# Performance work log

Measured on AMD Instinct MI355X. Metric: run time of the kernel, lower is better.

Reference implementation:

```python
import jax, jax.numpy as jnp
import numpy as np

B, L, E, D = 4, 2048, 512, 128


def setup_inputs() -> dict:
    key = jax.random.key(0)
    k1, k2 = jax.random.split(key)
    emb_sentences = jax.random.normal(k1, (B, L, E), dtype=jnp.float32)
    # torch nn.Linear weight layout: [out_dim, in_dim]
    W = jax.random.normal(k2, (D, E), dtype=jnp.float32) * (1.0 / np.sqrt(E))
    return {"emb_sentences": emb_sentences, "W": W}


def reference(emb_sentences, W):
    # dep_embeddings = Linear(emb) with no bias: [B, L, D]
    dep = jnp.einsum('ble,de->bld', emb_sentences, W)
    # All-pairs squared Euclidean distances without the O(L^2 * D)
    # broadcast intermediate: ||xi - xj||^2 = ||xi||^2 + ||xj||^2 - 2 xi.xj
    sq = jnp.sum(dep * dep, axis=-1)                 # [B, L]
    gram = jnp.einsum('bid,bjd->bij', dep, dep)      # [B, L, L]
    distances = sq[:, :, None] + sq[:, None, :] - 2.0 * gram
    return dep, distances
```

## Files before the change

### kernel.cpp

```cpp
#include <hip/hip_runtime.h>
#include <hip/hip_bf16.h>


typedef __attribute__((ext_vector_type(8))) short  short8;
typedef __attribute__((ext_vector_type(4))) float  floatx4;

#define B_  4
#define L_  2048
#define E_  512
#define D_  128
#define M_  (B_*L_)

__device__ __forceinline__ unsigned short f2bf(float x) {
    union { float f; unsigned u; } v; v.f = x;
    unsigned r = v.u + 0x7FFF + ((v.u >> 16) & 1);
    return (unsigned short)(r >> 16);
}

__global__ __launch_bounds__(256)
void kA(const float* __restrict__ emb, const float* __restrict__ W,
        float* __restrict__ dep_out, unsigned short* __restrict__ dep_b16)
{
    __shared__ __align__(16) unsigned short As[128][40];
    __shared__ __align__(16) unsigned short Bs[128][40];

    const int tid  = threadIdx.x;
    const int lane = tid & 63;
    const int wave = tid >> 6;
    const int wr = wave >> 1, wc = wave & 1;
    const int l15 = lane & 15, lg = lane >> 4;
    const long m0 = (long)blockIdx.x * 128;

    floatx4 acc[4][4];
    #pragma unroll
    for (int i = 0; i < 4; ++i)
        #pragma unroll
        for (int j = 0; j < 4; ++j)
            acc[i][j] = (floatx4){0.f, 0.f, 0.f, 0.f};

    for (int k0 = 0; k0 < E_; k0 += 32) {
        #pragma unroll
        for (int jj = 0; jj < 4; ++jj) {
            int chunk = tid + 256 * jj;
            int row = chunk >> 3, c4 = chunk & 7;
            float4 va = *reinterpret_cast<const float4*>(emb + (m0 + row) * E_ + k0 + c4 * 4);
            ushort4 ua;
            ua.x = f2bf(va.x); ua.y = f2bf(va.y); ua.z = f2bf(va.z); ua.w = f2bf(va.w);
            *reinterpret_cast<ushort4*>(&As[row][c4 * 4]) = ua;
            float4 vb = *reinterpret_cast<const float4*>(W + row * E_ + k0 + c4 * 4);
            ushort4 ub;
            ub.x = f2bf(vb.x); ub.y = f2bf(vb.y); ub.z = f2bf(vb.z); ub.w = f2bf(vb.w);
            *reinterpret_cast<ushort4*>(&Bs[row][c4 * 4]) = ub;
        }
        __syncthreads();

        short8 af[4], bfr[4];
        #pragma unroll
        for (int mi = 0; mi < 4; ++mi)
            af[mi] = *reinterpret_cast<const short8*>(&As[wr * 64 + mi * 16 + l15][lg * 8]);
        #pragma unroll
        for (int ni = 0; ni < 4; ++ni)
            bfr[ni] = *reinterpret_cast<const short8*>(&Bs[wc * 64 + ni * 16 + l15][lg * 8]);
        #pragma unroll
        for (int mi = 0; mi < 4; ++mi)
            #pragma unroll
            for (int ni = 0; ni < 4; ++ni)
                acc[mi][ni] = __builtin_amdgcn_mfma_f32_16x16x32_bf16(
                    af[mi], bfr[ni], acc[mi][ni], 0, 0, 0);
        __syncthreads();
    }

    #pragma unroll
    for (int mi = 0; mi < 4; ++mi) {
        #pragma unroll
        for (int j = 0; j < 4; ++j) {
            long row = m0 + wr * 64 + mi * 16 + lg * 4 + j;
            #pragma unroll
            for (int ni = 0; ni < 4; ++ni) {
                int col = wc * 64 + ni * 16 + l15;
                float v = acc[mi][ni][j];
                dep_out[row * D_ + col] = v;
                dep_b16[row * D_ + col] = f2bf(v);
            }
        }
    }
}

__global__ __launch_bounds__(256)
void kSQ(const unsigned short* __restrict__ dep_b16, float* __restrict__ sq)
{
    int row  = blockIdx.x * 4 + (threadIdx.x >> 6);
    int lane = threadIdx.x & 63;
    unsigned v = *reinterpret_cast<const unsigned*>(dep_b16 + (long)row * D_ + lane * 2);
    union { unsigned u; float f; } a, b;
    a.u = v << 16; b.u = v & 0xFFFF0000u;
    float s = a.f * a.f + b.f * b.f;
    #pragma unroll
    for (int off = 32; off; off >>= 1) s += __shfl_down(s, off);
    if (lane == 0) sq[row] = s;
}

__global__ __launch_bounds__(256)
void kB(const unsigned short* __restrict__ dep_b16, const float* __restrict__ sq,
        float* __restrict__ dist)
{
    __shared__ __align__(16) unsigned short Is[128][136];
    __shared__ __align__(16) unsigned short Js[128][136];

    const int tid  = threadIdx.x;
    const int lane = tid & 63;
    const int wave = tid >> 6;
    const int wr = wave >> 1, wc = wave & 1;
    const int l15 = lane & 15, lg = lane >> 4;
    const int b  = blockIdx.z;
    const int i0 = blockIdx.y * 128;
    const int j0 = blockIdx.x * 128;
    const unsigned short* depb = dep_b16 + (long)b * L_ * D_;

    #pragma unroll
    for (int jj = 0; jj < 8; ++jj) {
        int chunk = tid + 256 * jj;
        int row = chunk >> 4, c8 = chunk & 15;
        short8 vi = *reinterpret_cast<const short8*>(depb + (long)(i0 + row) * D_ + c8 * 8);
        *reinterpret_cast<short8*>(&Is[row][c8 * 8]) = vi;
        short8 vj = *reinterpret_cast<const short8*>(depb + (long)(j0 + row) * D_ + c8 * 8);
        *reinterpret_cast<short8*>(&Js[row][c8 * 8]) = vj;
    }
    __syncthreads();

    floatx4 acc[4][4];
    #pragma unroll
    for (int i = 0; i < 4; ++i)
        #pragma unroll
        for (int j = 0; j < 4; ++j)
            acc[i][j] = (floatx4){0.f, 0.f, 0.f, 0.f};

    #pragma unroll
    for (int kk = 0; kk < 4; ++kk) {
        short8 af[4], bfr[4];
        #pragma unroll
        for (int mi = 0; mi < 4; ++mi)
            af[mi] = *reinterpret_cast<const short8*>(&Is[wr * 64 + mi * 16 + l15][kk * 32 + lg * 8]);
        #pragma unroll
        for (int ni = 0; ni < 4; ++ni)
            bfr[ni] = *reinterpret_cast<const short8*>(&Js[wc * 64 + ni * 16 + l15][kk * 32 + lg * 8]);
        #pragma unroll
        for (int mi = 0; mi < 4; ++mi)
            #pragma unroll
            for (int ni = 0; ni < 4; ++ni)
                acc[mi][ni] = __builtin_amdgcn_mfma_f32_16x16x32_bf16(
                    af[mi], bfr[ni], acc[mi][ni], 0, 0, 0);
    }

    const float* sqb = sq + b * L_;
    float sqc[4];
    #pragma unroll
    for (int ni = 0; ni < 4; ++ni)
        sqc[ni] = sqb[j0 + wc * 64 + ni * 16 + l15];

    float* db = dist + (long)b * L_ * L_;
    #pragma unroll
    for (int mi = 0; mi < 4; ++mi) {
        #pragma unroll
        for (int j = 0; j < 4; ++j) {
            int row = i0 + wr * 64 + mi * 16 + lg * 4 + j;
            float sr = sqb[row];
            #pragma unroll
            for (int ni = 0; ni < 4; ++ni) {
                int col = j0 + wc * 64 + ni * 16 + l15;
                db[(long)row * L_ + col] = sr + sqc[ni] - 2.0f * acc[mi][ni][j];
            }
        }
    }
}

extern "C" void kernel_launch(void* const* d_in, const int* in_sizes, int n_in,
                              void* d_out, int out_size, void* d_ws, size_t ws_size,
                              hipStream_t stream)
{
    const float* emb = (const float*)d_in[0];
    const float* W   = (const float*)d_in[1];

    float* dep_out = (float*)d_out;
    float* dist    = dep_out + (size_t)M_ * D_;

    unsigned short* dep_b16 = (unsigned short*)d_ws;
    float* sq = (float*)((char*)d_ws + (size_t)M_ * D_ * sizeof(unsigned short));

    hipLaunchKernelGGL(kA,  dim3(M_ / 128), dim3(256), 0, stream, emb, W, dep_out, dep_b16);
    hipLaunchKernelGGL(kSQ, dim3(M_ / 4),   dim3(256), 0, stream, dep_b16, sq);
    hipLaunchKernelGGL(kB,  dim3(L_ / 128, L_ / 128, B_), dim3(256), 0, stream,
                       dep_b16, sq, dist);
}
```

Before: 45.56 us.

## Drop LDS staging in both GEMMs, pre-convert W to bf16, shrink kA tiles

Adds a small kernel that converts W to bf16 once per call. The projection GEMM now uses 32-row tiles (more blocks) and loads MFMA fragments straight from global memory into registers with no LDS or barriers. The gram kernel also drops its LDS staging and reads bf16 fragments directly from global memory, relying on the L1/L2 caches for reuse. This removes shared-memory traffic and synchronisation, at the cost of more redundant global loads, less coalesced access patterns and one extra kernel launch.

```diff
diff --git a/kernel.cpp b/kernel.cpp
--- a/kernel.cpp
+++ b/kernel.cpp
@@ -18,66 +18,70 @@
 }
 
 __global__ __launch_bounds__(256)
-void kA(const float* __restrict__ emb, const float* __restrict__ W,
+void kW(const float* __restrict__ W, unsigned short* __restrict__ Wb)
+{
+    int i = (blockIdx.x * 256 + threadIdx.x) * 4;
+    float4 v = *reinterpret_cast<const float4*>(W + i);
+    ushort4 u;
+    u.x = f2bf(v.x); u.y = f2bf(v.y); u.z = f2bf(v.z); u.w = f2bf(v.w);
+    *reinterpret_cast<ushort4*>(Wb + i) = u;
+}
+
+__global__ __launch_bounds__(256)
+void kA(const float* __restrict__ emb, const unsigned short* __restrict__ Wb,
         float* __restrict__ dep_out, unsigned short* __restrict__ dep_b16)
 {
-    __shared__ __align__(16) unsigned short As[128][40];
-    __shared__ __align__(16) unsigned short Bs[128][40];
+    const int lane = threadIdx.x & 63;
+    const int wave = threadIdx.x >> 6;
+    const int l15 = lane & 15, lg = lane >> 4;
+    const long m0 = (long)blockIdx.x * 32;
 
-    const int tid  = threadIdx.x;
-    const int lane = tid & 63;
-    const int wave = tid >> 6;
-    const int wr = wave >> 1, wc = wave & 1;
-    const int l15 = lane & 15, lg = lane >> 4;
-    const long m0 = (long)blockIdx.x * 128;
-
-    floatx4 acc[4][4];
+    floatx4 acc[2][2];
     #pragma unroll
-    for (int i = 0; i < 4; ++i)
+    for (int i = 0; i < 2; ++i)
         #pragma unroll
-        for (int j = 0; j < 4; ++j)
+        for (int j = 0; j < 2; ++j)
             acc[i][j] = (floatx4){0.f, 0.f, 0.f, 0.f};
 
+    const float* a0 = emb + (m0 + l15) * E_;
+    const float* a1 = emb + (m0 + 16 + l15) * E_;
+    const unsigned short* b0 = Wb + (wave * 32 + l15) * E_;
+    const unsigned short* b1 = Wb + (wave * 32 + 16 + l15) * E_;
+
+    #pragma unroll
     for (int k0 = 0; k0 < E_; k0 += 32) {
+        const int kc = k0 + lg * 8;
+        short8 af[2], bf[2];
         #pragma unroll
-        for (int jj = 0; jj < 4; ++jj) {
-            int chunk = tid + 256 * jj;
-            int row = chunk >> 3, c4 = chunk & 7;
-            float4 va = *reinterpret_cast<const float4*>(emb + (m0 + row) * E_ + k0 + c4 * 4);
-            ushort4 ua;
-            ua.x = f2bf(va.x); ua.y = f2bf(va.y); ua.z = f2bf(va.z); ua.w = f2bf(va.w);
-            *reinterpret_cast<ushort4*>(&As[row][c4 * 4]) = ua;
-            float4 vb = *reinterpret_cast<const float4*>(W + row * E_ + k0 + c4 * 4);
-            ushort4 ub;
-            ub.x = f2bf(vb.x); ub.y = f2bf(vb.y); ub.z = f2bf(vb.z); ub.w = f2bf(vb.w);
-            *reinterpret_cast<ushort4*>(&Bs[row][c4 * 4]) = ub;
+        for (int mi = 0; mi < 2; ++mi) {
+            const float* ap = (mi == 0 ? a0 : a1) + kc;
+            float4 x = *reinterpret_cast<const float4*>(ap);
+            float4 y = *reinterpret_cast<const float4*>(ap + 4);
+            short8 t;
+            t[0] = (short)f2bf(x.x); t[1] = (short)f2bf(x.y);
+            t[2] = (short)f2bf(x.z); t[3] = (short)f2bf(x.w);
+            t[4] = (short)f2bf(y.x); t[5] = (short)f2bf(y.y);
+            t[6] = (short)f2bf(y.z); t[7] = (short)f2bf(y.w);
+            af[mi] = t;
         }
-        __syncthreads();
-
-        short8 af[4], bfr[4];
+        bf[0] = *reinterpret_cast<const short8*>(b0 + kc);
+        bf[1] = *reinterpret_cast<const short8*>(b1 + kc);
         #pragma unroll
-        for (int mi = 0; mi < 4; ++mi)
-            af[mi] = *reinterpret_cast<const short8*>(&As[wr * 64 + mi * 16 + l15][lg * 8]);
-        #pragma unroll
-        for (int ni = 0; ni < 4; ++ni)
-            bfr[ni] = *reinterpret_cast<const short8*>(&Bs[wc * 64 + ni * 16 + l15][lg * 8]);
-        #pragma unroll
-        for (int mi = 0; mi < 4; ++mi)
+        for (int mi = 0; mi < 2; ++mi)
             #pragma unroll
-            for (int ni = 0; ni < 4; ++ni)
+            for (int ni = 0; ni < 2; ++ni)
                 acc[mi][ni] = __builtin_amdgcn_mfma_f32_16x16x32_bf16(
-                    af[mi], bfr[ni], acc[mi][ni], 0, 0, 0);
-        __syncthreads();
+                    af[mi], bf[ni], acc[mi][ni], 0, 0, 0);
     }
 
     #pragma unroll
-    for (int mi = 0; mi < 4; ++mi) {
+    for (int mi = 0; mi < 2; ++mi) {
         #pragma unroll
         for (int j = 0; j < 4; ++j) {
-            long row = m0 + wr * 64 + mi * 16 + lg * 4 + j;
+            long row = m0 + mi * 16 + lg * 4 + j;
             #pragma unroll
-            for (int ni = 0; ni < 4; ++ni) {
-                int col = wc * 64 + ni * 16 + l15;
+            for (int ni = 0; ni < 2; ++ni) {
+                int col = wave * 32 + ni * 16 + l15;
                 float v = acc[mi][ni][j];
                 dep_out[row * D_ + col] = v;
                 dep_b16[row * D_ + col] = f2bf(v);
@@ -104,9 +108,6 @@
 void kB(const unsigned short* __restrict__ dep_b16, const float* __restrict__ sq,
         float* __restrict__ dist)
 {
-    __shared__ __align__(16) unsigned short Is[128][136];
-    __shared__ __align__(16) unsigned short Js[128][136];
-
     const int tid  = threadIdx.x;
     const int lane = tid & 63;
     const int wave = tid >> 6;
@@ -117,17 +118,6 @@
     const int j0 = blockIdx.x * 128;
     const unsigned short* depb = dep_b16 + (long)b * L_ * D_;
 
-    #pragma unroll
-    for (int jj = 0; jj < 8; ++jj) {
-        int chunk = tid + 256 * jj;
-        int row = chunk >> 4, c8 = chunk & 15;
-        short8 vi = *reinterpret_cast<const short8*>(depb + (long)(i0 + row) * D_ + c8 * 8);
-        *reinterpret_cast<short8*>(&Is[row][c8 * 8]) = vi;
-        short8 vj = *reinterpret_cast<const short8*>(depb + (long)(j0 + row) * D_ + c8 * 8);
-        *reinterpret_cast<short8*>(&Js[row][c8 * 8]) = vj;
-    }
-    __syncthreads();
-
     floatx4 acc[4][4];
     #pragma unroll
     for (int i = 0; i < 4; ++i)
@@ -135,21 +125,25 @@
         for (int j = 0; j < 4; ++j)
             acc[i][j] = (floatx4){0.f, 0.f, 0.f, 0.f};
 
+    const unsigned short* ibase = depb + (long)(i0 + wr * 64 + l15) * D_;
+    const unsigned short* jbase = depb + (long)(j0 + wc * 64 + l15) * D_;
+
     #pragma unroll
     for (int kk = 0; kk < 4; ++kk) {
-        short8 af[4], bfr[4];
+        const int kc = kk * 32 + lg * 8;
+        short8 af[4], bf[4];
         #pragma unroll
         for (int mi = 0; mi < 4; ++mi)
-            af[mi] = *reinterpret_cast<const short8*>(&Is[wr * 64 + mi * 16 + l15][kk * 32 + lg * 8]);
+            af[mi] = *reinterpret_cast<const short8*>(ibase + (long)mi * 16 * D_ + kc);
         #pragma unroll
         for (int ni = 0; ni < 4; ++ni)
-            bfr[ni] = *reinterpret_cast<const short8*>(&Js[wc * 64 + ni * 16 + l15][kk * 32 + lg * 8]);
+            bf[ni] = *reinterpret_cast<const short8*>(jbase + (long)ni * 16 * D_ + kc);
         #pragma unroll
         for (int mi = 0; mi < 4; ++mi)
             #pragma unroll
             for (int ni = 0; ni < 4; ++ni)
                 acc[mi][ni] = __builtin_amdgcn_mfma_f32_16x16x32_bf16(
-                    af[mi], bfr[ni], acc[mi][ni], 0, 0, 0);
+                    af[mi], bf[ni], acc[mi][ni], 0, 0, 0);
     }
 
     const float* sqb = sq + b * L_;
@@ -185,10 +179,14 @@
     float* dist    = dep_out + (size_t)M_ * D_;
 
     unsigned short* dep_b16 = (unsigned short*)d_ws;
-    float* sq = (float*)((char*)d_ws + (size_t)M_ * D_ * sizeof(unsigned short));
+    float* sq  = (float*)((char*)d_ws + (size_t)M_ * D_ * sizeof(unsigned short));
+    unsigned short* Wb = (unsigned short*)((char*)d_ws
+                         + (size_t)M_ * D_ * sizeof(unsigned short)
+                         + (size_t)M_ * sizeof(float));
 
-    hipLaunchKernelGGL(kA,  dim3(M_ / 128), dim3(256), 0, stream, emb, W, dep_out, dep_b16);
-    hipLaunchKernelGGL(kSQ, dim3(M_ / 4),   dim3(256), 0, stream, dep_b16, sq);
+    hipLaunchKernelGGL(kW,  dim3((D_ * E_) / (256 * 4)), dim3(256), 0, stream, W, Wb);
+    hipLaunchKernelGGL(kA,  dim3(M_ / 32), dim3(256), 0, stream, emb, Wb, dep_out, dep_b16);
+    hipLaunchKernelGGL(kSQ, dim3(M_ / 4),  dim3(256), 0, stream, dep_b16, sq);
     hipLaunchKernelGGL(kB,  dim3(L_ / 128, L_ / 128, B_), dim3(256), 0, stream,
                        dep_b16, sq, dist);
 }
```

Result: slower. 51.69 us (+13.5%).

## Fuse projection, norms and distance GEMM into one cooperative persistent kernel

Applied to the files above, without the earlier changes.

Replaces the three separate launches with one cooperative kernel of 512 blocks. Phase one computes a 16-row projection tile per block straight from global memory without LDS staging and folds the squared-norm reduction into its epilogue. A grid-wide sync follows, after which each block computes two 128x128 distance tiles. The aim is to remove launch gaps and the separate norm kernel, at the cost of a grid barrier, lower per-block reuse in the projection, and a fallback two-kernel path if the cooperative launch fails.

```diff
diff --git a/kernel.cpp b/kernel.cpp
--- a/kernel.cpp
+++ b/kernel.cpp
@@ -1,5 +1,8 @@
 #include <hip/hip_runtime.h>
 #include <hip/hip_bf16.h>
+#include <hip/hip_cooperative_groups.h>
+
+namespace cg = cooperative_groups;
 
 
 typedef __attribute__((ext_vector_type(8))) short  short8;
@@ -10,26 +13,105 @@
 #define E_  512
 #define D_  128
 #define M_  (B_*L_)
-
-__device__ __forceinline__ unsigned short f2bf(float x) {
-    union { float f; unsigned u; } v; v.f = x;
-    unsigned r = v.u + 0x7FFF + ((v.u >> 16) & 1);
-    return (unsigned short)(r >> 16);
-}
-
-__global__ __launch_bounds__(256)
-void kA(const float* __restrict__ emb, const float* __restrict__ W,
-        float* __restrict__ dep_out, unsigned short* __restrict__ dep_b16)
-{
-    __shared__ __align__(16) unsigned short As[128][40];
-    __shared__ __align__(16) unsigned short Bs[128][40];
-
-    const int tid  = threadIdx.x;
-    const int lane = tid & 63;
-    const int wave = tid >> 6;
+#define NBLK 512
+
+__device__ __forceinline__ unsigned short f2bfu(float x) {
+    __hip_bfloat16 h = __float2bfloat16(x);
+    union { __hip_bfloat16 h; unsigned short u; } c; c.h = h; return c.u;
+}
+__device__ __forceinline__ float bfu2f(unsigned short u) {
+    union { unsigned u32; float f; } c; c.u32 = ((unsigned)u) << 16; return c.f;
+}
+__device__ __forceinline__ short8 cvt8(const float* p) {
+    float4 x = *reinterpret_cast<const float4*>(p);
+    float4 y = *reinterpret_cast<const float4*>(p + 4);
+    short8 t;
+    t[0] = (short)f2bfu(x.x); t[1] = (short)f2bfu(x.y);
+    t[2] = (short)f2bfu(x.z); t[3] = (short)f2bfu(x.w);
+    t[4] = (short)f2bfu(y.x); t[5] = (short)f2bfu(y.y);
+    t[6] = (short)f2bfu(y.z); t[7] = (short)f2bfu(y.w);
+    return t;
+}
+
+__device__ __forceinline__ void phase1(int bid, int tid,
+    const float* __restrict__ emb, const float* __restrict__ W,
+    float* __restrict__ dep_out, unsigned short* __restrict__ dep_b16,
+    float* __restrict__ sq, float* pws )
+{
+    const int lane = tid & 63, wave = tid >> 6;
+    const int l15 = lane & 15, lg = lane >> 4;
+    const long m0 = (long)bid * 16;
+
+    floatx4 acc[2] = { (floatx4){0.f,0.f,0.f,0.f}, (floatx4){0.f,0.f,0.f,0.f} };
+    const float* ar = emb + (m0 + l15) * E_;
+    const float* b0 = W + (wave * 32 + l15) * E_;
+    const float* b1 = W + (wave * 32 + 16 + l15) * E_;
+
+    #pragma unroll
+    for (int k0 = 0; k0 < E_; k0 += 32) {
+        const int kc = k0 + lg * 8;
+        short8 af  = cvt8(ar + kc);
+        short8 bf0 = cvt8(b0 + kc);
+        short8 bf1 = cvt8(b1 + kc);
+        acc[0] = __builtin_amdgcn_mfma_f32_16x16x32_bf16(af, bf0, acc[0], 0, 0, 0);
+        acc[1] = __builtin_amdgcn_mfma_f32_16x16x32_bf16(af, bf1, acc[1], 0, 0, 0);
+    }
+
+    float p[4] = {0.f, 0.f, 0.f, 0.f};
+    #pragma unroll
+    for (int ni = 0; ni < 2; ++ni) {
+        #pragma unroll
+        for (int j = 0; j < 4; ++j) {
+            float v = acc[ni][j];
+            unsigned short us = f2bfu(v);
+            long row = m0 + lg * 4 + j;
+            int  col = wave * 32 + ni * 16 + l15;
+            dep_out[row * D_ + col] = v;
+            dep_b16[row * D_ + col] = us;
+            float vb = bfu2f(us);
+            p[j] += vb * vb;
+        }
+    }
+    #pragma unroll
+    for (int j = 0; j < 4; ++j) {
+        #pragma unroll
+        for (int off = 1; off < 16; off <<= 1)
+            p[j] += __shfl_xor(p[j], off);
+    }
+    if (l15 == 0) {
+        #pragma unroll
+        for (int j = 0; j < 4; ++j)
+            pws[(lg * 4 + j) * 4 + wave] = p[j];
+    }
+    __syncthreads();
+    if (tid < 16)
+        sq[m0 + tid] = pws[tid * 4] + pws[tid * 4 + 1] + pws[tid * 4 + 2] + pws[tid * 4 + 3];
+}
+
+__device__ __forceinline__ void phase2(int t, int tid,
+    const unsigned short* __restrict__ dep_b16, const float* __restrict__ sq,
+    float* __restrict__ dist,
+    unsigned short (*Is)[136], unsigned short (*Js)[136])
+{
+    const int lane = tid & 63, wave = tid >> 6;
     const int wr = wave >> 1, wc = wave & 1;
     const int l15 = lane & 15, lg = lane >> 4;
-    const long m0 = (long)blockIdx.x * 128;
+    const int b  = t >> 8;
+    const int i0 = ((t >> 4) & 15) * 128;
+    const int j0 = (t & 15) * 128;
+    const unsigned short* depb = dep_b16 + (long)b * L_ * D_;
+
+    __syncthreads();
+    #pragma unroll
+    for (int jj = 0; jj < 8; ++jj) {
+        int chunk = tid + 256 * jj;
+        int row = chunk >> 4, c8 = chunk & 15;
+        *reinterpret_cast<short8*>(&Is[row][c8 * 8]) =
+            *reinterpret_cast<const short8*>(depb + (long)(i0 + row) * D_ + c8 * 8);
+        *reinterpret_cast<short8*>(&Js[row][c8 * 8]) =
+            *reinterpret_cast<const short8*>(depb + (long)(j0 + row) * D_ + c8 * 8);
+    }
+    __syncthreads();
 
     floatx4 acc[4][4];
     #pragma unroll
@@ -38,118 +120,21 @@
         for (int j = 0; j < 4; ++j)
             acc[i][j] = (floatx4){0.f, 0.f, 0.f, 0.f};
 
-    for (int k0 = 0; k0 < E_; k0 += 32) {
-        #pragma unroll
-        for (int jj = 0; jj < 4; ++jj) {
-            int chunk = tid + 256 * jj;
-            int row = chunk >> 3, c4 = chunk & 7;
-            float4 va = *reinterpret_cast<const float4*>(emb + (m0 + row) * E_ + k0 + c4 * 4);
-            ushort4 ua;
-            ua.x = f2bf(va.x); ua.y = f2bf(va.y); ua.z = f2bf(va.z); ua.w = f2bf(va.w);
-            *reinterpret_cast<ushort4*>(&As[row][c4 * 4]) = ua;
-            float4 vb = *reinterpret_cast<const float4*>(W + row * E_ + k0 + c4 * 4);
-            ushort4 ub;
-            ub.x = f2bf(vb.x); ub.y = f2bf(vb.y); ub.z = f2bf(vb.z); ub.w = f2bf(vb.w);
-            *reinterpret_cast<ushort4*>(&Bs[row][c4 * 4]) = ub;
-        }
-        __syncthreads();
-
-        short8 af[4], bfr[4];
+    #pragma unroll
+    for (int kk = 0; kk < 4; ++kk) {
+        short8 af[4], bf[4];
         #pragma unroll
         for (int mi = 0; mi < 4; ++mi)
-            af[mi] = *reinterpret_cast<const short8*>(&As[wr * 64 + mi * 16 + l15][lg * 8]);
+            af[mi] = *reinterpret_cast<const short8*>(&Is[wr * 64 + mi * 16 + l15][kk * 32 + lg * 8]);
         #pragma unroll
         for (int ni = 0; ni < 4; ++ni)
-            bfr[ni] = *reinterpret_cast<const short8*>(&Bs[wc * 64 + ni * 16 + l15][lg * 8]);
+            bf[ni] = *reinterpret_cast<const short8*>(&Js[wc * 64 + ni * 16 + l15][kk * 32 + lg * 8]);
         #pragma unroll
         for (int mi = 0; mi < 4; ++mi)
             #pragma unroll
             for (int ni = 0; ni < 4; ++ni)
                 acc[mi][ni] = __builtin_amdgcn_mfma_f32_16x16x32_bf16(
-                    af[mi], bfr[ni], acc[mi][ni], 0, 0, 0);
-        __syncthreads();
-    }
-
-    #pragma unroll
-    for (int mi = 0; mi < 4; ++mi) {
-        #pragma unroll
-        for (int j = 0; j < 4; ++j) {
-            long row = m0 + wr * 64 + mi * 16 + lg * 4 + j;
-            #pragma unroll
-            for (int ni = 0; ni < 4; ++ni) {
-                int col = wc * 64 + ni * 16 + l15;
-                float v = acc[mi][ni][j];
-                dep_out[row * D_ + col] = v;
-                dep_b16[row * D_ + col] = f2bf(v);
-            }
-        }
-    }
-}
-
-__global__ __launch_bounds__(256)
-void kSQ(const unsigned short* __restrict__ dep_b16, float* __restrict__ sq)
-{
-    int row  = blockIdx.x * 4 + (threadIdx.x >> 6);
-    int lane = threadIdx.x & 63;
-    unsigned v = *reinterpret_cast<const unsigned*>(dep_b16 + (long)row * D_ + lane * 2);
-    union { unsigned u; float f; } a, b;
-    a.u = v << 16; b.u = v & 0xFFFF0000u;
-    float s = a.f * a.f + b.f * b.f;
-    #pragma unroll
-    for (int off = 32; off; off >>= 1) s += __shfl_down(s, off);
-    if (lane == 0) sq[row] = s;
-}
-
-__global__ __launch_bounds__(256)
-void kB(const unsigned short* __restrict__ dep_b16, const float* __restrict__ sq,
-        float* __restrict__ dist)
-{
-    __shared__ __align__(16) unsigned short Is[128][136];
-    __shared__ __align__(16) unsigned short Js[128][136];
-
-    const int tid  = threadIdx.x;
-    const int lane = tid & 63;
-    const int wave = tid >> 6;
-    const int wr = wave >> 1, wc = wave & 1;
-    const int l15 = lane & 15, lg = lane >> 4;
-    const int b  = blockIdx.z;
-    const int i0 = blockIdx.y * 128;
-    const int j0 = blockIdx.x * 128;
-    const unsigned short* depb = dep_b16 + (long)b * L_ * D_;
-
-    #pragma unroll
-    for (int jj = 0; jj < 8; ++jj) {
-        int chunk = tid + 256 * jj;
-        int row = chunk >> 4, c8 = chunk & 15;
-        short8 vi = *reinterpret_cast<const short8*>(depb + (long)(i0 + row) * D_ + c8 * 8);
-        *reinterpret_cast<short8*>(&Is[row][c8 * 8]) = vi;
-        short8 vj = *reinterpret_cast<const short8*>(depb + (long)(j0 + row) * D_ + c8 * 8);
-        *reinterpret_cast<short8*>(&Js[row][c8 * 8]) = vj;
-    }
-    __syncthreads();
-
-    floatx4 acc[4][4];
-    #pragma unroll
-    for (int i = 0; i < 4; ++i)
-        #pragma unroll
-        for (int j = 0; j < 4; ++j)
-            acc[i][j] = (floatx4){0.f, 0.f, 0.f, 0.f};
-
-    #pragma unroll
-    for (int kk = 0; kk < 4; ++kk) {
-        short8 af[4], bfr[4];
-        #pragma unroll
-        for (int mi = 0; mi < 4; ++mi)
-            af[mi] = *reinterpret_cast<const short8*>(&Is[wr * 64 + mi * 16 + l15][kk * 32 + lg * 8]);
-        #pragma unroll
-        for (int ni = 0; ni < 4; ++ni)
-            bfr[ni] = *reinterpret_cast<const short8*>(&Js[wc * 64 + ni * 16 + l15][kk * 32 + lg * 8]);
-        #pragma unroll
-        for (int mi = 0; mi < 4; ++mi)
-            #pragma unroll
-            for (int ni = 0; ni < 4; ++ni)
-                acc[mi][ni] = __builtin_amdgcn_mfma_f32_16x16x32_bf16(
-                    af[mi], bfr[ni], acc[mi][ni], 0, 0, 0);
+                    af[mi], bf[ni], acc[mi][ni], 0, 0, 0);
     }
 
     const float* sqb = sq + b * L_;
@@ -174,6 +159,42 @@
     }
 }
 
+__global__ __launch_bounds__(256, 2)
+void kFused(const float* __restrict__ emb, const float* __restrict__ W,
+            float* __restrict__ dep_out, unsigned short* __restrict__ dep_b16,
+            float* __restrict__ sq, float* __restrict__ dist)
+{
+    __shared__ __align__(16) unsigned short Is[128][136];
+    __shared__ __align__(16) unsigned short Js[128][136];
+
+    const int bid = blockIdx.x, tid = threadIdx.x;
+    phase1(bid, tid, emb, W, dep_out, dep_b16, sq, reinterpret_cast<float*>(&Is[0][0]));
+
+    cg::this_grid().sync();
+
+    phase2(bid,        tid, dep_b16, sq, dist, Is, Js);
+    phase2(bid + NBLK, tid, dep_b16, sq, dist, Is, Js);
+}
+
+__global__ __launch_bounds__(256, 2)
+void kP1(const float* __restrict__ emb, const float* __restrict__ W,
+         float* __restrict__ dep_out, unsigned short* __restrict__ dep_b16,
+         float* __restrict__ sq)
+{
+    __shared__ float pws[64];
+    phase1(blockIdx.x, threadIdx.x, emb, W, dep_out, dep_b16, sq, pws);
+}
+
+__global__ __launch_bounds__(256, 2)
+void kP2(const unsigned short* __restrict__ dep_b16, const float* __restrict__ sq,
+         float* __restrict__ dist)
+{
+    __shared__ __align__(16) unsigned short Is[128][136];
+    __shared__ __align__(16) unsigned short Js[128][136];
+    phase2(blockIdx.x,        threadIdx.x, dep_b16, sq, dist, Is, Js);
+    phase2(blockIdx.x + NBLK, threadIdx.x, dep_b16, sq, dist, Is, Js);
+}
+
 extern "C" void kernel_launch(void* const* d_in, const int* in_sizes, int n_in,
                               void* d_out, int out_size, void* d_ws, size_t ws_size,
                               hipStream_t stream)
@@ -187,8 +208,15 @@
     unsigned short* dep_b16 = (unsigned short*)d_ws;
     float* sq = (float*)((char*)d_ws + (size_t)M_ * D_ * sizeof(unsigned short));
 
-    hipLaunchKernelGGL(kA,  dim3(M_ / 128), dim3(256), 0, stream, emb, W, dep_out, dep_b16);
-    hipLaunchKernelGGL(kSQ, dim3(M_ / 4),   dim3(256), 0, stream, dep_b16, sq);
-    hipLaunchKernelGGL(kB,  dim3(L_ / 128, L_ / 128, B_), dim3(256), 0, stream,
-                       dep_b16, sq, dist);
-}
+    void* args[6] = { (void*)&emb, (void*)&W, (void*)&dep_out,
+                      (void*)&dep_b16, (void*)&sq, (void*)&dist };
+    hipError_t err = hipLaunchCooperativeKernel((const void*)kFused,
+                                                dim3(NBLK), dim3(256),
+                                                args, 0, stream);
+    if (err != hipSuccess) {
+        hipLaunchKernelGGL(kP1, dim3(NBLK), dim3(256), 0, stream,
+                           emb, W, dep_out, dep_b16, sq);
+        hipLaunchKernelGGL(kP2, dim3(NBLK), dim3(256), 0, stream,
+                           dep_b16, sq, dist);
+    }
+}
```

Measured after the change: 99.10 us. 118% more time.
